# Performance work log

Measured on AMD Instinct MI355X. Metric: run time of the kernel, lower is better.

The kernel has to match this reference:

```python
import jax, jax.numpy as jnp
import numpy as np

N = 50000
E = 800000
D_IN = 128
HID = 128
L = 3


def setup_inputs() -> dict:
    key = jax.random.key(0)
    ks = jax.random.split(key, 16)
    s = 0.05
    return {
        "x": jax.random.normal(ks[0], (N, D_IN), jnp.float32),
        "edge_attr": jax.random.normal(ks[1], (E, 1), jnp.float32),
        "edge_index": jax.random.randint(ks[2], (2, E), 0, N, jnp.int64),
        # stacked per-layer GINEConv params (all layers have in=out=128)
        "Wl1": jax.random.normal(ks[3], (L, D_IN, HID), jnp.float32) * s,
        "bl1": jax.random.normal(ks[4], (L, HID), jnp.float32) * s,
        "Wl2": jax.random.normal(ks[5], (L, HID, HID), jnp.float32) * s,
        "bl2": jax.random.normal(ks[6], (L, HID), jnp.float32) * s,
        # edge_attr linear: edge_dim=1 -> in_channels of each layer's nn
        "We": jax.random.normal(ks[7], (L, 1, D_IN), jnp.float32) * s,
        "be": jax.random.normal(ks[8], (L, D_IN), jnp.float32) * s,
        # edge predictor MLP: Linear(2*HID, HID) -> ReLU -> (Dropout: eval) -> Linear(HID, 1)
        "Wp1": jax.random.normal(ks[9], (2 * HID, HID), jnp.float32) * s,
        "bp1": jax.random.normal(ks[10], (HID,), jnp.float32) * s,
        "Wp2": jax.random.normal(ks[11], (HID, 1), jnp.float32) * s,
        "bp2": jax.random.normal(ks[12], (1,), jnp.float32) * s,
    }


def reference(x, edge_attr, edge_index, Wl1, bl1, Wl2, bl2, We, be, Wp1, bp1, Wp2, bp2):
    src, dst = edge_index[0], edge_index[1]  # PyG: row=source j, col=target i
    n = x.shape[0]
    for l in range(Wl1.shape[0]):
        # GINEConv message: ReLU(x_j + Lin(edge_attr)); sum-aggregate into target i
        msg = jax.nn.relu(x[src] + edge_attr @ We[l] + be[l])        # [E, D]
        aggr = jax.ops.segment_sum(msg, dst, num_segments=n)         # [N, D]
        # out = nn((1+eps)*x + aggr), eps=0; nn = Lin->ReLU->Lin; then outer ReLU
        h = jax.nn.relu((x + aggr) @ Wl1[l] + bl1[l])
        x = jax.nn.relu(h @ Wl2[l] + bl2[l])
    edge_feat = jnp.concatenate([x[src], x[dst]], axis=1)            # [E, 2*HID]
    h = jax.nn.relu(edge_feat @ Wp1 + bp1)                           # dropout = identity (eval)
    return (h @ Wp2 + bp2).squeeze(-1)                               # [E]
```

## Files before the change

kernel.cpp:

```cpp
#include <hip/hip_runtime.h>

#define NN 50000
#define NE 800000
#define DD 128

typedef __attribute__((ext_vector_type(8))) short short8;
typedef __attribute__((ext_vector_type(4))) float f32x4;

__device__ inline unsigned short f2bf_rne(float f) {
  unsigned u = __float_as_uint(f);
  u += 0x7FFF + ((u >> 16) & 1);
  return (unsigned short)(u >> 16);
}
__device__ inline float bf2f(unsigned short h) {
  return __uint_as_float(((unsigned)h) << 16);
}

__global__ __launch_bounds__(256) void prologue(
    const float* __restrict__ Wl1, const float* __restrict__ Wl2,
    const float* __restrict__ Wp1,
    unsigned short* __restrict__ WTh, unsigned short* __restrict__ WTl,
    const float2* __restrict__ xin2, unsigned* __restrict__ xbf2,
    int* __restrict__ cnt) {
  const int tid = blockIdx.x * 256 + threadIdx.x;
  if (tid < NN) cnt[tid] = 0;
  if (tid < 8 * 16384) {
    const int g = tid >> 14, idx = tid & 16383;
    const int n = idx >> 7, k = idx & 127;
    const float* s;
    if (g < 3) s = Wl1 + (size_t)g * 16384;
    else if (g < 6) s = Wl2 + (size_t)(g - 3) * 16384;
    else s = Wp1 + (size_t)(g - 6) * 16384;
    const float v = s[k * 128 + n];
    const unsigned short hi = f2bf_rne(v);
    WTh[tid] = hi;
    WTl[tid] = f2bf_rne(v - bf2f(hi));
  }
  if (tid < NN * DD / 2) {
    const float2 v = xin2[tid];
    xbf2[tid] = (unsigned)f2bf_rne(v.x) | ((unsigned)f2bf_rne(v.y) << 16);
  }
}

__global__ __launch_bounds__(256) void hist_rank(const int* __restrict__ dst,
                                                 int* __restrict__ cnt,
                                                 int* __restrict__ rank) {
  int e = blockIdx.x * 256 + threadIdx.x;
  if (e < NE) rank[e] = atomicAdd(&cnt[dst[e]], 1);
}

__global__ __launch_bounds__(1024) void scan_nodes(const int* __restrict__ cnt,
                                                   int* __restrict__ offs) {
  __shared__ int wsum[16];
  __shared__ int wpre[16];
  const int t = threadIdx.x;
  const int lane = t & 63, wv = t >> 6;
  int carry = 0;
  for (int base = 0; base < NN; base += 8192) {
    const int i0 = base + t * 8;
    int4 a = make_int4(0, 0, 0, 0), b = make_int4(0, 0, 0, 0);
    if (i0 + 8 <= NN) {
      a = *(const int4*)(cnt + i0);
      b = *(const int4*)(cnt + i0 + 4);
    } else if (i0 < NN) {
      int tmp[8];
      for (int j = 0; j < 8; ++j) tmp[j] = (i0 + j < NN) ? cnt[i0 + j] : 0;
      a = make_int4(tmp[0], tmp[1], tmp[2], tmp[3]);
      b = make_int4(tmp[4], tmp[5], tmp[6], tmp[7]);
    }
    const int own = a.x + a.y + a.z + a.w + b.x + b.y + b.z + b.w;
    int inc = own;
#pragma unroll
    for (int d = 1; d < 64; d <<= 1) {
      int v = __shfl_up(inc, d, 64);
      if (lane >= d) inc += v;
    }
    if (lane == 63) wsum[wv] = inc;
    __syncthreads();
    if (t < 16) {
      int v = wsum[t];
      int p = v;
#pragma unroll
      for (int d = 1; d < 16; d <<= 1) {
        int u = __shfl_up(p, d, 16);
        if (t >= d) p += u;
      }
      wpre[t] = p - v;
      if (t == 15) wsum[15] = p;
    }
    __syncthreads();
    int run = carry + wpre[wv] + inc - own;
    const int o0 = run,      o1 = o0 + a.x, o2 = o1 + a.y, o3 = o2 + a.z;
    const int o4 = o3 + a.w, o5 = o4 + b.x, o6 = o5 + b.y, o7 = o6 + b.z;
    if (i0 + 8 <= NN) {
      *(int4*)(offs + i0)     = make_int4(o0, o1, o2, o3);
      *(int4*)(offs + i0 + 4) = make_int4(o4, o5, o6, o7);
    } else if (i0 < NN) {
      const int o[8] = {o0, o1, o2, o3, o4, o5, o6, o7};
      for (int j = 0; j < 8; ++j)
        if (i0 + j < NN) offs[i0 + j] = o[j];
    }
    carry += wsum[15];
    __syncthreads();
  }
  if (t == 0) offs[NN] = carry;
}

__global__ __launch_bounds__(256) void csr_fill(
    const int* __restrict__ src, const int* __restrict__ dst,
    const float* __restrict__ ea, const int* __restrict__ offs,
    const int* __restrict__ rank, int4* __restrict__ recs) {
  int e = blockIdx.x * 256 + threadIdx.x;
  if (e >= NE) return;
  int pos = offs[dst[e]] + rank[e];
  recs[pos] = make_int4(src[e], e, __float_as_int(ea[e]), 0);
}

__global__ __launch_bounds__(256) void aggregate(
    const unsigned short* __restrict__ xbf,
    const int* __restrict__ offs, const int4* __restrict__ recs,
    const float4* __restrict__ We4, const float4* __restrict__ be4,
    float* __restrict__ out) {
  const int slot = threadIdx.x >> 5, lane = threadIdx.x & 31;
  const int n = blockIdx.x * 8 + slot;
  if (n >= NN) return;
  const float4 wv = We4[lane], bv = be4[lane];
  const uint2 sq = *(const uint2*)(xbf + (size_t)n * DD + lane * 4);
  float4 a0, a1, a2, a3;
  a0.x = __uint_as_float(sq.x << 16);
  a0.y = __uint_as_float(sq.x & 0xffff0000u);
  a0.z = __uint_as_float(sq.y << 16);
  a0.w = __uint_as_float(sq.y & 0xffff0000u);
  a1 = make_float4(0.f, 0.f, 0.f, 0.f);
  a2 = make_float4(0.f, 0.f, 0.f, 0.f);
  a3 = make_float4(0.f, 0.f, 0.f, 0.f);
  const int beg = offs[n], end = offs[n + 1];
  int i = beg;
#define ACCQ(acc, rec, qq)                                                    \
  {                                                                           \
    const float ee = __int_as_float((rec).z);                                 \
    const float g0 = __uint_as_float((qq).x << 16);                           \
    const float g1 = __uint_as_float((qq).x & 0xffff0000u);                   \
    const float g2 = __uint_as_float((qq).y << 16);                           \
    const float g3 = __uint_as_float((qq).y & 0xffff0000u);                   \
    acc.x += fmaxf(fmaf(ee, wv.x, bv.x) + g0, 0.f);                           \
    acc.y += fmaxf(fmaf(ee, wv.y, bv.y) + g1, 0.f);                           \
    acc.z += fmaxf(fmaf(ee, wv.z, bv.z) + g2, 0.f);                           \
    acc.w += fmaxf(fmaf(ee, wv.w, bv.w) + g3, 0.f);                           \
  }
  for (; i + 8 <= end; i += 8) {
    int4 r[8];
#pragma unroll
    for (int u = 0; u < 8; ++u) r[u] = recs[i + u];
    uint2 q[8];
#pragma unroll
    for (int u = 0; u < 8; ++u)
      q[u] = *(const uint2*)(xbf + (size_t)r[u].x * DD + lane * 4);
    ACCQ(a0, r[0], q[0]) ACCQ(a1, r[1], q[1]) ACCQ(a2, r[2], q[2]) ACCQ(a3, r[3], q[3])
    ACCQ(a0, r[4], q[4]) ACCQ(a1, r[5], q[5]) ACCQ(a2, r[6], q[6]) ACCQ(a3, r[7], q[7])
  }
  for (; i + 4 <= end; i += 4) {
    int4 r[4];
#pragma unroll
    for (int u = 0; u < 4; ++u) r[u] = recs[i + u];
    uint2 q[4];
#pragma unroll
    for (int u = 0; u < 4; ++u)
      q[u] = *(const uint2*)(xbf + (size_t)r[u].x * DD + lane * 4);
    ACCQ(a0, r[0], q[0]) ACCQ(a1, r[1], q[1]) ACCQ(a2, r[2], q[2]) ACCQ(a3, r[3], q[3])
  }
  for (; i < end; ++i) {
    const int4 r0 = recs[i];
    const uint2 q0 = *(const uint2*)(xbf + (size_t)r0.x * DD + lane * 4);
    ACCQ(a0, r0, q0)
  }
#undef ACCQ
  a0.x += a1.x + a2.x + a3.x;
  a0.y += a1.y + a2.y + a3.y;
  a0.z += a1.z + a2.z + a3.z;
  a0.w += a1.w + a2.w + a3.w;
  ((float4*)(out + (size_t)n * DD))[lane] = a0;
}

template <bool F32OUT, bool BFOUT>
__global__ __launch_bounds__(256) void fused_mlp(
    const float* __restrict__ in,
    const unsigned short* __restrict__ W1h, const unsigned short* __restrict__ W1l,
    const unsigned short* __restrict__ W2h, const unsigned short* __restrict__ W2l,
    const float* __restrict__ b1, const float* __restrict__ b2,
    float* __restrict__ out, unsigned short* __restrict__ outbf) {
  __shared__ float hl[16][132];
  const int t = threadIdx.x;
  const int w = t >> 6, l = t & 63;
  const int lr = l & 15, kg = l >> 4;

  short8 B1h_[2][4], B1l_[2][4], B2h_[2][4], B2l_[2][4];
#pragma unroll
  for (int ct = 0; ct < 2; ++ct)
#pragma unroll
    for (int ks = 0; ks < 4; ++ks) {
      const size_t bo = (size_t)((w * 2 + ct) * 16 + lr) * DD + ks * 32 + kg * 8;
      B1h_[ct][ks] = *(const short8*)(W1h + bo);
      B1l_[ct][ks] = *(const short8*)(W1l + bo);
      B2h_[ct][ks] = *(const short8*)(W2h + bo);
      B2l_[ct][ks] = *(const short8*)(W2l + bo);
    }
  const float b1v0 = b1[(w * 2 + 0) * 16 + lr];
  const float b1v1 = b1[(w * 2 + 1) * 16 + lr];
  const float b2v0 = b2[(w * 2 + 0) * 16 + lr];
  const float b2v1 = b2[(w * 2 + 1) * 16 + lr];

  for (int c = blockIdx.x; c < NN / 16; c += gridDim.x) {
    f32x4 acc[2];
    {
      const float* ap = in + ((size_t)c * 16 + lr) * DD + kg * 8;
      float va[4][8];
#pragma unroll
      for (int ks = 0; ks < 4; ++ks) {
        *(float4*)&va[ks][0] = *(const float4*)(ap + ks * 32);
        *(float4*)&va[ks][4] = *(const float4*)(ap + ks * 32 + 4);
      }
      short8 ah[4], al[4];
#pragma unroll
      for (int ks = 0; ks < 4; ++ks)
#pragma unroll
        for (int j = 0; j < 8; ++j) {
          unsigned short h = f2bf_rne(va[ks][j]);
          ah[ks][j] = (short)h;
          al[ks][j] = (short)f2bf_rne(va[ks][j] - bf2f(h));
        }
      acc[0] = (f32x4){0.f, 0.f, 0.f, 0.f};
      acc[1] = (f32x4){0.f, 0.f, 0.f, 0.f};
#pragma unroll
      for (int ks = 0; ks < 4; ++ks)
#pragma unroll
        for (int ct = 0; ct < 2; ++ct) {
          acc[ct] = __builtin_amdgcn_mfma_f32_16x16x32_bf16(ah[ks], B1h_[ct][ks], acc[ct], 0, 0, 0);
          acc[ct] = __builtin_amdgcn_mfma_f32_16x16x32_bf16(ah[ks], B1l_[ct][ks], acc[ct], 0, 0, 0);
          acc[ct] = __builtin_amdgcn_mfma_f32_16x16x32_bf16(al[ks], B1h_[ct][ks], acc[ct], 0, 0, 0);
        }
    }
    __syncthreads();
#pragma unroll
    for (int ct = 0; ct < 2; ++ct) {
      const float bb = ct ? b1v1 : b1v0;
      const int col = (w * 2 + ct) * 16 + lr;
#pragma unroll
      for (int q = 0; q < 4; ++q)
        hl[kg * 4 + q][col] = fmaxf(acc[ct][q] + bb, 0.f);
    }
    __syncthreads();
    {
      float va[4][8];
#pragma unroll
      for (int ks = 0; ks < 4; ++ks) {
        *(float4*)&va[ks][0] = *(const float4*)&hl[lr][ks * 32 + kg * 8];
        *(float4*)&va[ks][4] = *(const float4*)&hl[lr][ks * 32 + kg * 8 + 4];
      }
      short8 ah[4], al[4];
#pragma unroll
      for (int ks = 0; ks < 4; ++ks)
#pragma unroll
        for (int j = 0; j < 8; ++j) {
          unsigned short h = f2bf_rne(va[ks][j]);
          ah[ks][j] = (short)h;
          al[ks][j] = (short)f2bf_rne(va[ks][j] - bf2f(h));
        }
      acc[0] = (f32x4){0.f, 0.f, 0.f, 0.f};
      acc[1] = (f32x4){0.f, 0.f, 0.f, 0.f};
#pragma unroll
      for (int ks = 0; ks < 4; ++ks)
#pragma unroll
        for (int ct = 0; ct < 2; ++ct) {
          acc[ct] = __builtin_amdgcn_mfma_f32_16x16x32_bf16(ah[ks], B2h_[ct][ks], acc[ct], 0, 0, 0);
          acc[ct] = __builtin_amdgcn_mfma_f32_16x16x32_bf16(ah[ks], B2l_[ct][ks], acc[ct], 0, 0, 0);
          acc[ct] = __builtin_amdgcn_mfma_f32_16x16x32_bf16(al[ks], B2h_[ct][ks], acc[ct], 0, 0, 0);
        }
    }
#pragma unroll
    for (int ct = 0; ct < 2; ++ct) {
      const float bb = ct ? b2v1 : b2v0;
      const int col = (w * 2 + ct) * 16 + lr;
#pragma unroll
      for (int q = 0; q < 4; ++q) {
        const float v = fmaxf(acc[ct][q] + bb, 0.f);
        const size_t r = (size_t)c * 16 + kg * 4 + q;
        if (F32OUT) out[r * DD + col] = v;
        if (BFOUT) outbf[r * DD + col] = f2bf_rne(v);
      }
    }
  }
}

__global__ __launch_bounds__(256) void gemm_pred2(
    const float* __restrict__ in,
    const unsigned short* __restrict__ W1h, const unsigned short* __restrict__ W1l,
    const unsigned short* __restrict__ W2h, const unsigned short* __restrict__ W2l,
    const float* __restrict__ bp1,
    unsigned short* __restrict__ P1bf, unsigned short* __restrict__ P2bf) {
  const int t = threadIdx.x;
  const int w = t >> 6, l = t & 63;
  const int lr = l & 15, kg = l >> 4;

  short8 B1h[2][4], B1l[2][4], B2h[2][4], B2l[2][4];
#pragma unroll
  for (int ct = 0; ct < 2; ++ct)
#pragma unroll
    for (int ks = 0; ks < 4; ++ks) {
      const size_t bo = (size_t)((w * 2 + ct) * 16 + lr) * DD + ks * 32 + kg * 8;
      B1h[ct][ks] = *(const short8*)(W1h + bo);
      B1l[ct][ks] = *(const short8*)(W1l + bo);
      B2h[ct][ks] = *(const short8*)(W2h + bo);
      B2l[ct][ks] = *(const short8*)(W2l + bo);
    }
  float bv0 = bp1[(w * 2 + 0) * 16 + lr];
  float bv1 = bp1[(w * 2 + 1) * 16 + lr];

  for (int c = blockIdx.x; c < NN / 16; c += gridDim.x) {
    const float* ap = in + ((size_t)c * 16 + lr) * DD + kg * 8;
    float va[4][8];
#pragma unroll
    for (int ks = 0; ks < 4; ++ks) {
      *(float4*)&va[ks][0] = *(const float4*)(ap + ks * 32);
      *(float4*)&va[ks][4] = *(const float4*)(ap + ks * 32 + 4);
    }
    short8 ah[4], al[4];
#pragma unroll
    for (int ks = 0; ks < 4; ++ks)
#pragma unroll
      for (int j = 0; j < 8; ++j) {
        unsigned short h = f2bf_rne(va[ks][j]);
        ah[ks][j] = (short)h;
        al[ks][j] = (short)f2bf_rne(va[ks][j] - bf2f(h));
      }
    f32x4 acc1[2], acc2[2];
    acc1[0] = (f32x4){0.f, 0.f, 0.f, 0.f};
    acc1[1] = (f32x4){0.f, 0.f, 0.f, 0.f};
    acc2[0] = (f32x4){0.f, 0.f, 0.f, 0.f};
    acc2[1] = (f32x4){0.f, 0.f, 0.f, 0.f};
#pragma unroll
    for (int ks = 0; ks < 4; ++ks) {
#pragma unroll
      for (int ct = 0; ct < 2; ++ct) {
        acc1[ct] = __builtin_amdgcn_mfma_f32_16x16x32_bf16(ah[ks], B1h[ct][ks], acc1[ct], 0, 0, 0);
        acc1[ct] = __builtin_amdgcn_mfma_f32_16x16x32_bf16(ah[ks], B1l[ct][ks], acc1[ct], 0, 0, 0);
        acc1[ct] = __builtin_amdgcn_mfma_f32_16x16x32_bf16(al[ks], B1h[ct][ks], acc1[ct], 0, 0, 0);
        acc2[ct] = __builtin_amdgcn_mfma_f32_16x16x32_bf16(ah[ks], B2h[ct][ks], acc2[ct], 0, 0, 0);
        acc2[ct] = __builtin_amdgcn_mfma_f32_16x16x32_bf16(ah[ks], B2l[ct][ks], acc2[ct], 0, 0, 0);
        acc2[ct] = __builtin_amdgcn_mfma_f32_16x16x32_bf16(al[ks], B2h[ct][ks], acc2[ct], 0, 0, 0);
      }
    }
#pragma unroll
    for (int ct = 0; ct < 2; ++ct) {
      const int col = (w * 2 + ct) * 16 + lr;
      const float bb = ct ? bv1 : bv0;
#pragma unroll
      for (int q4 = 0; q4 < 4; ++q4) {
        const size_t r = (size_t)c * 16 + kg * 4 + q4;
        P1bf[r * DD + col] = f2bf_rne(acc1[ct][q4]);
        P2bf[r * DD + col] = f2bf_rne(acc2[ct][q4] + bb);
      }
    }
  }
}

__global__ __launch_bounds__(256) void edge_out(
    const unsigned short* __restrict__ P1bf, const unsigned short* __restrict__ P2bf,
    const int* __restrict__ offs, const int4* __restrict__ recs,
    const float4* __restrict__ Wp2_4,
    const float* __restrict__ bp2, float* __restrict__ out) {
  const int slot = threadIdx.x >> 5, lane = threadIdx.x & 31;
  const int n = blockIdx.x * 8 + slot;
  if (n >= NN) return;
  const float4 w = Wp2_4[lane];
  const float bb = bp2[0];
  const uint2 pq = *(const uint2*)(P2bf + (size_t)n * DD + lane * 4);
  float4 p2;
  p2.x = __uint_as_float(pq.x << 16);
  p2.y = __uint_as_float(pq.x & 0xffff0000u);
  p2.z = __uint_as_float(pq.y << 16);
  p2.w = __uint_as_float(pq.y & 0xffff0000u);
  const int beg = offs[n], end = offs[n + 1];
  int i = beg;
#define EDGEV(vv, qq)                                                         \
  {                                                                           \
    const float q0 = __uint_as_float((qq).x << 16);                           \
    const float q1 = __uint_as_float((qq).x & 0xffff0000u);                   \
    const float q2 = __uint_as_float((qq).y << 16);                           \
    const float q3 = __uint_as_float((qq).y & 0xffff0000u);                   \
    vv = fmaxf(q0 + p2.x, 0.f) * w.x + fmaxf(q1 + p2.y, 0.f) * w.y            \
       + fmaxf(q2 + p2.z, 0.f) * w.z + fmaxf(q3 + p2.w, 0.f) * w.w;           \
  }
  for (; i + 8 <= end; i += 8) {
    int4 r[8];
#pragma unroll
    for (int u = 0; u < 8; ++u) r[u] = recs[i + u];
    uint2 q[8];
#pragma unroll
    for (int u = 0; u < 8; ++u)
      q[u] = *(const uint2*)(P1bf + (size_t)r[u].x * DD + lane * 4);
    float v[8];
#pragma unroll
    for (int u = 0; u < 8; ++u) EDGEV(v[u], q[u])
#pragma unroll
    for (int m = 16; m >= 1; m >>= 1) {
#pragma unroll
      for (int u = 0; u < 8; ++u) v[u] += __shfl_xor(v[u], m, 64);
    }
    if (lane == 0) {
#pragma unroll
      for (int u = 0; u < 8; ++u) out[r[u].y] = v[u] + bb;
    }
  }
  for (; i + 4 <= end; i += 4) {
    int4 r[4];
#pragma unroll
    for (int u = 0; u < 4; ++u) r[u] = recs[i + u];
    uint2 q[4];
#pragma unroll
    for (int u = 0; u < 4; ++u)
      q[u] = *(const uint2*)(P1bf + (size_t)r[u].x * DD + lane * 4);
    float v[4];
#pragma unroll
    for (int u = 0; u < 4; ++u) EDGEV(v[u], q[u])
#pragma unroll
    for (int m = 16; m >= 1; m >>= 1) {
#pragma unroll
      for (int u = 0; u < 4; ++u) v[u] += __shfl_xor(v[u], m, 64);
    }
    if (lane == 0) {
#pragma unroll
      for (int u = 0; u < 4; ++u) out[r[u].y] = v[u] + bb;
    }
  }
  for (; i < end; ++i) {
    const int4 rec = recs[i];
    const uint2 qq = *(const uint2*)(P1bf + (size_t)rec.x * DD + lane * 4);
    float v;
    EDGEV(v, qq)
#pragma unroll
    for (int m = 16; m >= 1; m >>= 1) v += __shfl_xor(v, m, 64);
    if (lane == 0) out[rec.y] = v + bb;
  }
#undef EDGEV
}

extern "C" void kernel_launch(void* const* d_in, const int* in_sizes, int n_in,
                              void* d_out, int out_size, void* d_ws, size_t ws_size,
                              hipStream_t stream) {
  const float* x_in = (const float*)d_in[0];
  const float* ea   = (const float*)d_in[1];
  const int*   ei   = (const int*)d_in[2];
  const float* Wl1 = (const float*)d_in[3];
  const float* bl1 = (const float*)d_in[4];
  const float* Wl2 = (const float*)d_in[5];
  const float* bl2 = (const float*)d_in[6];
  const float* We  = (const float*)d_in[7];
  const float* be  = (const float*)d_in[8];
  const float* Wp1 = (const float*)d_in[9];
  const float* bp1 = (const float*)d_in[10];
  const float* Wp2 = (const float*)d_in[11];
  const float* bp2 = (const float*)d_in[12];
  const int* src = ei;
  const int* dst = ei + NE;

  float* bufA   = (float*)d_ws;
  float* bufB   = bufA + (size_t)NN * DD;
  int*   cnt    = (int*)(bufB + (size_t)NN * DD);
  int*   offs   = cnt + NN;
  int*   rank   = offs + NN + 1;
  int4*  recs   = (int4*)(((uintptr_t)(rank + NE) + 15) & ~(uintptr_t)15);
  unsigned short* WTh = (unsigned short*)(recs + NE);
  unsigned short* WTl = WTh + 8 * 16384;
  unsigned short* xbf = WTl + 8 * 16384;

  prologue<<<(NN * DD / 2 + 255) / 256, 256, 0, stream>>>(
      Wl1, Wl2, Wp1, WTh, WTl, (const float2*)x_in, (unsigned*)xbf, cnt);
  hist_rank<<<NE / 256, 256, 0, stream>>>(dst, cnt, rank);
  scan_nodes<<<1, 1024, 0, stream>>>(cnt, offs);
  csr_fill<<<NE / 256, 256, 0, stream>>>(src, dst, ea, offs, rank, recs);

  const int GB = 1024;
  const int AB = (NN + 7) / 8;
#define WH(g) (WTh + (size_t)(g) * 16384)
#define WL(g) (WTl + (size_t)(g) * 16384)

  aggregate<<<AB, 256, 0, stream>>>(
      xbf, offs, recs, (const float4*)We, (const float4*)be, bufA);
  fused_mlp<false, true><<<GB, 256, 0, stream>>>(
      bufA, WH(0), WL(0), WH(3), WL(3), bl1, bl2, nullptr, xbf);
  aggregate<<<AB, 256, 0, stream>>>(
      xbf, offs, recs, (const float4*)(We + DD), (const float4*)(be + DD), bufA);
  fused_mlp<false, true><<<GB, 256, 0, stream>>>(
      bufA, WH(1), WL(1), WH(4), WL(4), bl1 + DD, bl2 + DD, nullptr, xbf);
  aggregate<<<AB, 256, 0, stream>>>(
      xbf, offs, recs, (const float4*)(We + 2 * DD), (const float4*)(be + 2 * DD), bufA);
  fused_mlp<true, false><<<GB, 256, 0, stream>>>(
      bufA, WH(2), WL(2), WH(5), WL(5), bl1 + 2 * DD, bl2 + 2 * DD, bufB, nullptr);
  gemm_pred2<<<GB, 256, 0, stream>>>(bufB, WH(6), WL(6), WH(7), WL(7), bp1,
                                     (unsigned short*)bufA, xbf);
  edge_out<<<AB, 256, 0, stream>>>(
      (const unsigned short*)bufA, xbf, offs, recs,
      (const float4*)Wp2, bp2, (float*)d_out);
}
```

Baseline: 386.1 us.

## Pack CSR records into 8 bytes and gather rows with 16-lane, 16-byte loads

Shrinks each CSR record from an int4 to a uint2. The record packs a 16-bit source index, a 32-bit edge id split across both words, and the edge attribute rounded to bf16. This halves the record traffic read by the three aggregate passes and by edge_out. Both gather kernels also now map 16 lanes per node with 128-bit loads instead of 32 lanes with 64-bit loads, so each block handles 16 nodes and edge_out needs a shorter shuffle reduction. In exchange, the edge attribute loses precision, and the packing relies on N fitting in 16 bits.

Measured after the change: 390.0 us. About the same (+1.0%).

```diff
diff --git a/kernel.cpp b/kernel.cpp
--- a/kernel.cpp
+++ b/kernel.cpp
@@ -15,6 +15,8 @@
 __device__ inline float bf2f(unsigned short h) {
   return __uint_as_float(((unsigned)h) << 16);
 }
+__device__ inline float bflo(unsigned u) { return __uint_as_float(u << 16); }
+__device__ inline float bfhi(unsigned u) { return __uint_as_float(u & 0xffff0000u); }
 
 __global__ __launch_bounds__(256) void prologue(
     const float* __restrict__ Wl1, const float* __restrict__ Wl2,
@@ -109,77 +111,79 @@
 __global__ __launch_bounds__(256) void csr_fill(
     const int* __restrict__ src, const int* __restrict__ dst,
     const float* __restrict__ ea, const int* __restrict__ offs,
-    const int* __restrict__ rank, int4* __restrict__ recs) {
+    const int* __restrict__ rank, uint2* __restrict__ recs) {
   int e = blockIdx.x * 256 + threadIdx.x;
   if (e >= NE) return;
   int pos = offs[dst[e]] + rank[e];
-  recs[pos] = make_int4(src[e], e, __float_as_int(ea[e]), 0);
+  const unsigned s = (unsigned)src[e];
+  const unsigned eb = (unsigned)f2bf_rne(ea[e]);
+  recs[pos] = make_uint2(s | ((unsigned)e << 16),
+                         ((unsigned)e >> 16) | (eb << 16));
 }
 
 __global__ __launch_bounds__(256) void aggregate(
     const unsigned short* __restrict__ xbf,
-    const int* __restrict__ offs, const int4* __restrict__ recs,
+    const int* __restrict__ offs, const uint2* __restrict__ recs,
     const float4* __restrict__ We4, const float4* __restrict__ be4,
     float* __restrict__ out) {
-  const int slot = threadIdx.x >> 5, lane = threadIdx.x & 31;
-  const int n = blockIdx.x * 8 + slot;
+  const int slot = threadIdx.x >> 4, lane = threadIdx.x & 15;
+  const int n = blockIdx.x * 16 + slot;
   if (n >= NN) return;
-  const float4 wv = We4[lane], bv = be4[lane];
-  const uint2 sq = *(const uint2*)(xbf + (size_t)n * DD + lane * 4);
-  float4 a0, a1, a2, a3;
-  a0.x = __uint_as_float(sq.x << 16);
-  a0.y = __uint_as_float(sq.x & 0xffff0000u);
-  a0.z = __uint_as_float(sq.y << 16);
-  a0.w = __uint_as_float(sq.y & 0xffff0000u);
-  a1 = make_float4(0.f, 0.f, 0.f, 0.f);
-  a2 = make_float4(0.f, 0.f, 0.f, 0.f);
-  a3 = make_float4(0.f, 0.f, 0.f, 0.f);
+  const float4 wv0 = We4[lane * 2], wv1 = We4[lane * 2 + 1];
+  const float4 bv0 = be4[lane * 2], bv1 = be4[lane * 2 + 1];
+  float acc[8];
+  {
+    const uint4 sq = *(const uint4*)(xbf + (size_t)n * DD + lane * 8);
+    acc[0] = bflo(sq.x); acc[1] = bfhi(sq.x);
+    acc[2] = bflo(sq.y); acc[3] = bfhi(sq.y);
+    acc[4] = bflo(sq.z); acc[5] = bfhi(sq.z);
+    acc[6] = bflo(sq.w); acc[7] = bfhi(sq.w);
+  }
   const int beg = offs[n], end = offs[n + 1];
   int i = beg;
-#define ACCQ(acc, rec, qq)                                                    \
+#define ACC8(rec, q)                                                          \
   {                                                                           \
-    const float ee = __int_as_float((rec).z);                                 \
-    const float g0 = __uint_as_float((qq).x << 16);                           \
-    const float g1 = __uint_as_float((qq).x & 0xffff0000u);                   \
-    const float g2 = __uint_as_float((qq).y << 16);                           \
-    const float g3 = __uint_as_float((qq).y & 0xffff0000u);                   \
-    acc.x += fmaxf(fmaf(ee, wv.x, bv.x) + g0, 0.f);                           \
-    acc.y += fmaxf(fmaf(ee, wv.y, bv.y) + g1, 0.f);                           \
-    acc.z += fmaxf(fmaf(ee, wv.z, bv.z) + g2, 0.f);                           \
-    acc.w += fmaxf(fmaf(ee, wv.w, bv.w) + g3, 0.f);                           \
+    const float ee = bf2f((unsigned short)((rec).y >> 16));                   \
+    acc[0] += fmaxf(fmaf(ee, wv0.x, bv0.x) + bflo((q).x), 0.f);               \
+    acc[1] += fmaxf(fmaf(ee, wv0.y, bv0.y) + bfhi((q).x), 0.f);               \
+    acc[2] += fmaxf(fmaf(ee, wv0.z, bv0.z) + bflo((q).y), 0.f);               \
+    acc[3] += fmaxf(fmaf(ee, wv0.w, bv0.w) + bfhi((q).y), 0.f);               \
+    acc[4] += fmaxf(fmaf(ee, wv1.x, bv1.x) + bflo((q).z), 0.f);               \
+    acc[5] += fmaxf(fmaf(ee, wv1.y, bv1.y) + bfhi((q).z), 0.f);               \
+    acc[6] += fmaxf(fmaf(ee, wv1.z, bv1.z) + bflo((q).w), 0.f);               \
+    acc[7] += fmaxf(fmaf(ee, wv1.w, bv1.w) + bfhi((q).w), 0.f);               \
   }
   for (; i + 8 <= end; i += 8) {
-    int4 r[8];
+    uint2 r[8];
 #pragma unroll
     for (int u = 0; u < 8; ++u) r[u] = recs[i + u];
-    uint2 q[8];
+    uint4 q[8];
 #pragma unroll
     for (int u = 0; u < 8; ++u)
-      q[u] = *(const uint2*)(xbf + (size_t)r[u].x * DD + lane * 4);
-    ACCQ(a0, r[0], q[0]) ACCQ(a1, r[1], q[1]) ACCQ(a2, r[2], q[2]) ACCQ(a3, r[3], q[3])
-    ACCQ(a0, r[4], q[4]) ACCQ(a1, r[5], q[5]) ACCQ(a2, r[6], q[6]) ACCQ(a3, r[7], q[7])
+      q[u] = *(const uint4*)(xbf + (size_t)(r[u].x & 0xFFFFu) * DD + lane * 8);
+#pragma unroll
+    for (int u = 0; u < 8; ++u) ACC8(r[u], q[u])
   }
   for (; i + 4 <= end; i += 4) {
-    int4 r[4];
+    uint2 r[4];
 #pragma unroll
     for (int u = 0; u < 4; ++u) r[u] = recs[i + u];
-    uint2 q[4];
+    uint4 q[4];
 #pragma unroll
     for (int u = 0; u < 4; ++u)
-      q[u] = *(const uint2*)(xbf + (size_t)r[u].x * DD + lane * 4);
-    ACCQ(a0, r[0], q[0]) ACCQ(a1, r[1], q[1]) ACCQ(a2, r[2], q[2]) ACCQ(a3, r[3], q[3])
+      q[u] = *(const uint4*)(xbf + (size_t)(r[u].x & 0xFFFFu) * DD + lane * 8);
+#pragma unroll
+    for (int u = 0; u < 4; ++u) ACC8(r[u], q[u])
   }
   for (; i < end; ++i) {
-    const int4 r0 = recs[i];
-    const uint2 q0 = *(const uint2*)(xbf + (size_t)r0.x * DD + lane * 4);
-    ACCQ(a0, r0, q0)
-  }
-#undef ACCQ
-  a0.x += a1.x + a2.x + a3.x;
-  a0.y += a1.y + a2.y + a3.y;
-  a0.z += a1.z + a2.z + a3.z;
-  a0.w += a1.w + a2.w + a3.w;
-  ((float4*)(out + (size_t)n * DD))[lane] = a0;
+    const uint2 r0 = recs[i];
+    const uint4 q0 = *(const uint4*)(xbf + (size_t)(r0.x & 0xFFFFu) * DD + lane * 8);
+    ACC8(r0, q0)
+  }
+#undef ACC8
+  float* orow = out + (size_t)n * DD + lane * 8;
+  *(float4*)orow = make_float4(acc[0], acc[1], acc[2], acc[3]);
+  *(float4*)(orow + 4) = make_float4(acc[4], acc[5], acc[6], acc[7]);
 }
 
 template <bool F32OUT, bool BFOUT>
@@ -366,83 +370,89 @@
 
 __global__ __launch_bounds__(256) void edge_out(
     const unsigned short* __restrict__ P1bf, const unsigned short* __restrict__ P2bf,
-    const int* __restrict__ offs, const int4* __restrict__ recs,
+    const int* __restrict__ offs, const uint2* __restrict__ recs,
     const float4* __restrict__ Wp2_4,
     const float* __restrict__ bp2, float* __restrict__ out) {
-  const int slot = threadIdx.x >> 5, lane = threadIdx.x & 31;
-  const int n = blockIdx.x * 8 + slot;
+  const int slot = threadIdx.x >> 4, lane = threadIdx.x & 15;
+  const int n = blockIdx.x * 16 + slot;
   if (n >= NN) return;
-  const float4 w = Wp2_4[lane];
+  const float4 w0 = Wp2_4[lane * 2], w1 = Wp2_4[lane * 2 + 1];
   const float bb = bp2[0];
-  const uint2 pq = *(const uint2*)(P2bf + (size_t)n * DD + lane * 4);
-  float4 p2;
-  p2.x = __uint_as_float(pq.x << 16);
-  p2.y = __uint_as_float(pq.x & 0xffff0000u);
-  p2.z = __uint_as_float(pq.y << 16);
-  p2.w = __uint_as_float(pq.y & 0xffff0000u);
+  float p[8];
+  {
+    const uint4 pq = *(const uint4*)(P2bf + (size_t)n * DD + lane * 8);
+    p[0] = bflo(pq.x); p[1] = bfhi(pq.x);
+    p[2] = bflo(pq.y); p[3] = bfhi(pq.y);
+    p[4] = bflo(pq.z); p[5] = bfhi(pq.z);
+    p[6] = bflo(pq.w); p[7] = bfhi(pq.w);
+  }
   const int beg = offs[n], end = offs[n + 1];
   int i = beg;
-#define EDGEV(vv, qq)                                                         \
+#define EDGEV(vv, q)                                                          \
   {                                                                           \
-    const float q0 = __uint_as_float((qq).x << 16);                           \
-    const float q1 = __uint_as_float((qq).x & 0xffff0000u);                   \
-    const float q2 = __uint_as_float((qq).y << 16);                           \
-    const float q3 = __uint_as_float((qq).y & 0xffff0000u);                   \
-    vv = fmaxf(q0 + p2.x, 0.f) * w.x + fmaxf(q1 + p2.y, 0.f) * w.y            \
-       + fmaxf(q2 + p2.z, 0.f) * w.z + fmaxf(q3 + p2.w, 0.f) * w.w;           \
-  }
+    vv = fmaxf(bflo((q).x) + p[0], 0.f) * w0.x                                \
+       + fmaxf(bfhi((q).x) + p[1], 0.f) * w0.y                                \
+       + fmaxf(bflo((q).y) + p[2], 0.f) * w0.z                                \
+       + fmaxf(bfhi((q).y) + p[3], 0.f) * w0.w                                \
+       + fmaxf(bflo((q).z) + p[4], 0.f) * w1.x                                \
+       + fmaxf(bfhi((q).z) + p[5], 0.f) * w1.y                                \
+       + fmaxf(bflo((q).w) + p[6], 0.f) * w1.z                                \
+       + fmaxf(bfhi((q).w) + p[7], 0.f) * w1.w;                               \
+  }
+#define EID(r) (((r).x >> 16) | (((r).y & 0xFFFFu) << 16))
   for (; i + 8 <= end; i += 8) {
-    int4 r[8];
+    uint2 r[8];
 #pragma unroll
     for (int u = 0; u < 8; ++u) r[u] = recs[i + u];
-    uint2 q[8];
+    uint4 q[8];
 #pragma unroll
     for (int u = 0; u < 8; ++u)
-      q[u] = *(const uint2*)(P1bf + (size_t)r[u].x * DD + lane * 4);
+      q[u] = *(const uint4*)(P1bf + (size_t)(r[u].x & 0xFFFFu) * DD + lane * 8);
     float v[8];
 #pragma unroll
     for (int u = 0; u < 8; ++u) EDGEV(v[u], q[u])
 #pragma unroll
-    for (int m = 16; m >= 1; m >>= 1) {
+    for (int m = 8; m >= 1; m >>= 1) {
 #pragma unroll
       for (int u = 0; u < 8; ++u) v[u] += __shfl_xor(v[u], m, 64);
     }
     if (lane == 0) {
 #pragma unroll
-      for (int u = 0; u < 8; ++u) out[r[u].y] = v[u] + bb;
+      for (int u = 0; u < 8; ++u) out[EID(r[u])] = v[u] + bb;
     }
   }
   for (; i + 4 <= end; i += 4) {
-    int4 r[4];
+    uint2 r[4];
 #pragma unroll
     for (int u = 0; u < 4; ++u) r[u] = recs[i + u];
-    uint2 q[4];
+    uint4 q[4];
 #pragma unroll
     for (int u = 0; u < 4; ++u)
-      q[u] = *(const uint2*)(P1bf + (size_t)r[u].x * DD + lane * 4);
+      q[u] = *(const uint4*)(P1bf + (size_t)(r[u].x & 0xFFFFu) * DD + lane * 8);
     float v[4];
 #pragma unroll
     for (int u = 0; u < 4; ++u) EDGEV(v[u], q[u])
 #pragma unroll
-    for (int m = 16; m >= 1; m >>= 1) {
+    for (int m = 8; m >= 1; m >>= 1) {
 #pragma unroll
       for (int u = 0; u < 4; ++u) v[u] += __shfl_xor(v[u], m, 64);
     }
     if (lane == 0) {
 #pragma unroll
-      for (int u = 0; u < 4; ++u) out[r[u].y] = v[u] + bb;
+      for (int u = 0; u < 4; ++u) out[EID(r[u])] = v[u] + bb;
     }
   }
   for (; i < end; ++i) {
-    const int4 rec = recs[i];
-    const uint2 qq = *(const uint2*)(P1bf + (size_t)rec.x * DD + lane * 4);
+    const uint2 r0 = recs[i];
+    const uint4 q0 = *(const uint4*)(P1bf + (size_t)(r0.x & 0xFFFFu) * DD + lane * 8);
     float v;
-    EDGEV(v, qq)
-#pragma unroll
-    for (int m = 16; m >= 1; m >>= 1) v += __shfl_xor(v, m, 64);
-    if (lane == 0) out[rec.y] = v + bb;
+    EDGEV(v, q0)
+#pragma unroll
+    for (int m = 8; m >= 1; m >>= 1) v += __shfl_xor(v, m, 64);
+    if (lane == 0) out[EID(r0)] = v + bb;
   }
 #undef EDGEV
+#undef EID
 }
 
 extern "C" void kernel_launch(void* const* d_in, const int* in_sizes, int n_in,
@@ -469,7 +479,7 @@
   int*   cnt    = (int*)(bufB + (size_t)NN * DD);
   int*   offs   = cnt + NN;
   int*   rank   = offs + NN + 1;
-  int4*  recs   = (int4*)(((uintptr_t)(rank + NE) + 15) & ~(uintptr_t)15);
+  uint2* recs   = (uint2*)(((uintptr_t)(rank + NE) + 15) & ~(uintptr_t)15);
   unsigned short* WTh = (unsigned short*)(recs + NE);
   unsigned short* WTl = WTh + 8 * 16384;
   unsigned short* xbf = WTl + 8 * 16384;
@@ -481,7 +491,7 @@
   csr_fill<<<NE / 256, 256, 0, stream>>>(src, dst, ea, offs, rank, recs);
 
   const int GB = 1024;
-  const int AB = (NN + 7) / 8;
+  const int AB = (NN + 15) / 16;
 #define WH(g) (WTh + (size_t)(g) * 16384)
 #define WL(g) (WTl + (size_t)(g) * 16384)
 
```

## Pack CSR records to 8 bytes and store aggregates and activations as bf16

Applied to the files above, without the earlier changes.

CSR records shrink from int4 to uint2, packing a 16-bit source index, a 32-bit edge id split across both words, and the bf16 edge attribute. Aggregate outputs and the final-layer activations are now written as bf16, so the MLP and predictor GEMMs load bf16 directly. This drops the hi/lo split of activations and one of the three MFMA passes per split-precision product. The aim is to cut memory traffic and MFMA work, at the cost of precision. The 16-bit source field only holds because N=50000 fits in 16 bits, and it truncates larger node ids.

Measured after the change: 355.6 us. 1.09x faster.

```diff
diff --git a/kernel.cpp b/kernel.cpp
--- a/kernel.cpp
+++ b/kernel.cpp
@@ -15,6 +15,8 @@
 __device__ inline float bf2f(unsigned short h) {
   return __uint_as_float(((unsigned)h) << 16);
 }
+__device__ inline float bflo(unsigned u) { return __uint_as_float(u << 16); }
+__device__ inline float bfhi(unsigned u) { return __uint_as_float(u & 0xffff0000u); }
 
 __global__ __launch_bounds__(256) void prologue(
     const float* __restrict__ Wl1, const float* __restrict__ Wl2,
@@ -109,28 +111,31 @@
 __global__ __launch_bounds__(256) void csr_fill(
     const int* __restrict__ src, const int* __restrict__ dst,
     const float* __restrict__ ea, const int* __restrict__ offs,
-    const int* __restrict__ rank, int4* __restrict__ recs) {
+    const int* __restrict__ rank, uint2* __restrict__ recs) {
   int e = blockIdx.x * 256 + threadIdx.x;
   if (e >= NE) return;
   int pos = offs[dst[e]] + rank[e];
-  recs[pos] = make_int4(src[e], e, __float_as_int(ea[e]), 0);
+  const unsigned s = (unsigned)src[e];
+  const unsigned eb = (unsigned)f2bf_rne(ea[e]);
+  recs[pos] = make_uint2(s | ((unsigned)e << 16),
+                         ((unsigned)e >> 16) | (eb << 16));
 }
 
 __global__ __launch_bounds__(256) void aggregate(
     const unsigned short* __restrict__ xbf,
-    const int* __restrict__ offs, const int4* __restrict__ recs,
+    const int* __restrict__ offs, const uint2* __restrict__ recs,
     const float4* __restrict__ We4, const float4* __restrict__ be4,
-    float* __restrict__ out) {
+    unsigned* __restrict__ outbf2) {
   const int slot = threadIdx.x >> 5, lane = threadIdx.x & 31;
   const int n = blockIdx.x * 8 + slot;
   if (n >= NN) return;
   const float4 wv = We4[lane], bv = be4[lane];
-  const uint2 sq = *(const uint2*)(xbf + (size_t)n * DD + lane * 4);
   float4 a0, a1, a2, a3;
-  a0.x = __uint_as_float(sq.x << 16);
-  a0.y = __uint_as_float(sq.x & 0xffff0000u);
-  a0.z = __uint_as_float(sq.y << 16);
-  a0.w = __uint_as_float(sq.y & 0xffff0000u);
+  {
+    const uint2 sq = *(const uint2*)(xbf + (size_t)n * DD + lane * 4);
+    a0.x = bflo(sq.x); a0.y = bfhi(sq.x);
+    a0.z = bflo(sq.y); a0.w = bfhi(sq.y);
+  }
   a1 = make_float4(0.f, 0.f, 0.f, 0.f);
   a2 = make_float4(0.f, 0.f, 0.f, 0.f);
   a3 = make_float4(0.f, 0.f, 0.f, 0.f);
@@ -138,40 +143,36 @@
   int i = beg;
 #define ACCQ(acc, rec, qq)                                                    \
   {                                                                           \
-    const float ee = __int_as_float((rec).z);                                 \
-    const float g0 = __uint_as_float((qq).x << 16);                           \
-    const float g1 = __uint_as_float((qq).x & 0xffff0000u);                   \
-    const float g2 = __uint_as_float((qq).y << 16);                           \
-    const float g3 = __uint_as_float((qq).y & 0xffff0000u);                   \
-    acc.x += fmaxf(fmaf(ee, wv.x, bv.x) + g0, 0.f);                           \
-    acc.y += fmaxf(fmaf(ee, wv.y, bv.y) + g1, 0.f);                           \
-    acc.z += fmaxf(fmaf(ee, wv.z, bv.z) + g2, 0.f);                           \
-    acc.w += fmaxf(fmaf(ee, wv.w, bv.w) + g3, 0.f);                           \
+    const float ee = bf2f((unsigned short)((rec).y >> 16));                   \
+    acc.x += fmaxf(fmaf(ee, wv.x, bv.x) + bflo((qq).x), 0.f);                 \
+    acc.y += fmaxf(fmaf(ee, wv.y, bv.y) + bfhi((qq).x), 0.f);                 \
+    acc.z += fmaxf(fmaf(ee, wv.z, bv.z) + bflo((qq).y), 0.f);                 \
+    acc.w += fmaxf(fmaf(ee, wv.w, bv.w) + bfhi((qq).y), 0.f);                 \
   }
   for (; i + 8 <= end; i += 8) {
-    int4 r[8];
+    uint2 r[8];
 #pragma unroll
     for (int u = 0; u < 8; ++u) r[u] = recs[i + u];
     uint2 q[8];
 #pragma unroll
     for (int u = 0; u < 8; ++u)
-      q[u] = *(const uint2*)(xbf + (size_t)r[u].x * DD + lane * 4);
+      q[u] = *(const uint2*)(xbf + (size_t)(r[u].x & 0xFFFFu) * DD + lane * 4);
     ACCQ(a0, r[0], q[0]) ACCQ(a1, r[1], q[1]) ACCQ(a2, r[2], q[2]) ACCQ(a3, r[3], q[3])
     ACCQ(a0, r[4], q[4]) ACCQ(a1, r[5], q[5]) ACCQ(a2, r[6], q[6]) ACCQ(a3, r[7], q[7])
   }
   for (; i + 4 <= end; i += 4) {
-    int4 r[4];
+    uint2 r[4];
 #pragma unroll
     for (int u = 0; u < 4; ++u) r[u] = recs[i + u];
     uint2 q[4];
 #pragma unroll
     for (int u = 0; u < 4; ++u)
-      q[u] = *(const uint2*)(xbf + (size_t)r[u].x * DD + lane * 4);
+      q[u] = *(const uint2*)(xbf + (size_t)(r[u].x & 0xFFFFu) * DD + lane * 4);
     ACCQ(a0, r[0], q[0]) ACCQ(a1, r[1], q[1]) ACCQ(a2, r[2], q[2]) ACCQ(a3, r[3], q[3])
   }
   for (; i < end; ++i) {
-    const int4 r0 = recs[i];
-    const uint2 q0 = *(const uint2*)(xbf + (size_t)r0.x * DD + lane * 4);
+    const uint2 r0 = recs[i];
+    const uint2 q0 = *(const uint2*)(xbf + (size_t)(r0.x & 0xFFFFu) * DD + lane * 4);
     ACCQ(a0, r0, q0)
   }
 #undef ACCQ
@@ -179,16 +180,18 @@
   a0.y += a1.y + a2.y + a3.y;
   a0.z += a1.z + a2.z + a3.z;
   a0.w += a1.w + a2.w + a3.w;
-  ((float4*)(out + (size_t)n * DD))[lane] = a0;
-}
-
-template <bool F32OUT, bool BFOUT>
+  const unsigned lo = (unsigned)f2bf_rne(a0.x) | ((unsigned)f2bf_rne(a0.y) << 16);
+  const unsigned hi = (unsigned)f2bf_rne(a0.z) | ((unsigned)f2bf_rne(a0.w) << 16);
+  uint2* orow = (uint2*)(outbf2 + (size_t)n * (DD / 2)) + lane;
+  *orow = make_uint2(lo, hi);
+}
+
 __global__ __launch_bounds__(256) void fused_mlp(
-    const float* __restrict__ in,
+    const unsigned short* __restrict__ in,
     const unsigned short* __restrict__ W1h, const unsigned short* __restrict__ W1l,
     const unsigned short* __restrict__ W2h, const unsigned short* __restrict__ W2l,
     const float* __restrict__ b1, const float* __restrict__ b2,
-    float* __restrict__ out, unsigned short* __restrict__ outbf) {
+    unsigned short* __restrict__ outbf) {
   __shared__ float hl[16][132];
   const int t = threadIdx.x;
   const int w = t >> 6, l = t & 63;
@@ -213,12 +216,36 @@
   for (int c = blockIdx.x; c < NN / 16; c += gridDim.x) {
     f32x4 acc[2];
     {
-      const float* ap = in + ((size_t)c * 16 + lr) * DD + kg * 8;
+      const unsigned short* ap = in + ((size_t)c * 16 + lr) * DD + kg * 8;
+      short8 ah[4];
+#pragma unroll
+      for (int ks = 0; ks < 4; ++ks) ah[ks] = *(const short8*)(ap + ks * 32);
+      acc[0] = (f32x4){0.f, 0.f, 0.f, 0.f};
+      acc[1] = (f32x4){0.f, 0.f, 0.f, 0.f};
+#pragma unroll
+      for (int ks = 0; ks < 4; ++ks)
+#pragma unroll
+        for (int ct = 0; ct < 2; ++ct) {
+          acc[ct] = __builtin_amdgcn_mfma_f32_16x16x32_bf16(ah[ks], B1h_[ct][ks], acc[ct], 0, 0, 0);
+          acc[ct] = __builtin_amdgcn_mfma_f32_16x16x32_bf16(ah[ks], B1l_[ct][ks], acc[ct], 0, 0, 0);
+        }
+    }
+    __syncthreads();
+#pragma unroll
+    for (int ct = 0; ct < 2; ++ct) {
+      const float bb = ct ? b1v1 : b1v0;
+      const int col = (w * 2 + ct) * 16 + lr;
+#pragma unroll
+      for (int q = 0; q < 4; ++q)
+        hl[kg * 4 + q][col] = fmaxf(acc[ct][q] + bb, 0.f);
+    }
+    __syncthreads();
+    {
       float va[4][8];
 #pragma unroll
       for (int ks = 0; ks < 4; ++ks) {
-        *(float4*)&va[ks][0] = *(const float4*)(ap + ks * 32);
-        *(float4*)&va[ks][4] = *(const float4*)(ap + ks * 32 + 4);
+        *(float4*)&va[ks][0] = *(const float4*)&hl[lr][ks * 32 + kg * 8];
+        *(float4*)&va[ks][4] = *(const float4*)&hl[lr][ks * 32 + kg * 8 + 4];
       }
       short8 ah[4], al[4];
 #pragma unroll
@@ -235,43 +262,6 @@
       for (int ks = 0; ks < 4; ++ks)
 #pragma unroll
         for (int ct = 0; ct < 2; ++ct) {
-          acc[ct] = __builtin_amdgcn_mfma_f32_16x16x32_bf16(ah[ks], B1h_[ct][ks], acc[ct], 0, 0, 0);
-          acc[ct] = __builtin_amdgcn_mfma_f32_16x16x32_bf16(ah[ks], B1l_[ct][ks], acc[ct], 0, 0, 0);
-          acc[ct] = __builtin_amdgcn_mfma_f32_16x16x32_bf16(al[ks], B1h_[ct][ks], acc[ct], 0, 0, 0);
-        }
-    }
-    __syncthreads();
-#pragma unroll
-    for (int ct = 0; ct < 2; ++ct) {
-      const float bb = ct ? b1v1 : b1v0;
-      const int col = (w * 2 + ct) * 16 + lr;
-#pragma unroll
-      for (int q = 0; q < 4; ++q)
-        hl[kg * 4 + q][col] = fmaxf(acc[ct][q] + bb, 0.f);
-    }
-    __syncthreads();
-    {
-      float va[4][8];
-#pragma unroll
-      for (int ks = 0; ks < 4; ++ks) {
-        *(float4*)&va[ks][0] = *(const float4*)&hl[lr][ks * 32 + kg * 8];
-        *(float4*)&va[ks][4] = *(const float4*)&hl[lr][ks * 32 + kg * 8 + 4];
-      }
-      short8 ah[4], al[4];
-#pragma unroll
-      for (int ks = 0; ks < 4; ++ks)
-#pragma unroll
-        for (int j = 0; j < 8; ++j) {
-          unsigned short h = f2bf_rne(va[ks][j]);
-          ah[ks][j] = (short)h;
-          al[ks][j] = (short)f2bf_rne(va[ks][j] - bf2f(h));
-        }
-      acc[0] = (f32x4){0.f, 0.f, 0.f, 0.f};
-      acc[1] = (f32x4){0.f, 0.f, 0.f, 0.f};
-#pragma unroll
-      for (int ks = 0; ks < 4; ++ks)
-#pragma unroll
-        for (int ct = 0; ct < 2; ++ct) {
           acc[ct] = __builtin_amdgcn_mfma_f32_16x16x32_bf16(ah[ks], B2h_[ct][ks], acc[ct], 0, 0, 0);
           acc[ct] = __builtin_amdgcn_mfma_f32_16x16x32_bf16(ah[ks], B2l_[ct][ks], acc[ct], 0, 0, 0);
           acc[ct] = __builtin_amdgcn_mfma_f32_16x16x32_bf16(al[ks], B2h_[ct][ks], acc[ct], 0, 0, 0);
@@ -284,16 +274,14 @@
 #pragma unroll
       for (int q = 0; q < 4; ++q) {
         const float v = fmaxf(acc[ct][q] + bb, 0.f);
-        const size_t r = (size_t)c * 16 + kg * 4 + q;
-        if (F32OUT) out[r * DD + col] = v;
-        if (BFOUT) outbf[r * DD + col] = f2bf_rne(v);
+        outbf[((size_t)c * 16 + kg * 4 + q) * DD + col] = f2bf_rne(v);
       }
     }
   }
 }
 
 __global__ __launch_bounds__(256) void gemm_pred2(
-    const float* __restrict__ in,
+    const unsigned short* __restrict__ in,
     const unsigned short* __restrict__ W1h, const unsigned short* __restrict__ W1l,
     const unsigned short* __restrict__ W2h, const unsigned short* __restrict__ W2l,
     const float* __restrict__ bp1,
@@ -317,22 +305,10 @@
   float bv1 = bp1[(w * 2 + 1) * 16 + lr];
 
   for (int c = blockIdx.x; c < NN / 16; c += gridDim.x) {
-    const float* ap = in + ((size_t)c * 16 + lr) * DD + kg * 8;
-    float va[4][8];
-#pragma unroll
-    for (int ks = 0; ks < 4; ++ks) {
-      *(float4*)&va[ks][0] = *(const float4*)(ap + ks * 32);
-      *(float4*)&va[ks][4] = *(const float4*)(ap + ks * 32 + 4);
-    }
-    short8 ah[4], al[4];
-#pragma unroll
-    for (int ks = 0; ks < 4; ++ks)
-#pragma unroll
-      for (int j = 0; j < 8; ++j) {
-        unsigned short h = f2bf_rne(va[ks][j]);
-        ah[ks][j] = (short)h;
-        al[ks][j] = (short)f2bf_rne(va[ks][j] - bf2f(h));
-      }
+    const unsigned short* ap = in + ((size_t)c * 16 + lr) * DD + kg * 8;
+    short8 ah[4];
+#pragma unroll
+    for (int ks = 0; ks < 4; ++ks) ah[ks] = *(const short8*)(ap + ks * 32);
     f32x4 acc1[2], acc2[2];
     acc1[0] = (f32x4){0.f, 0.f, 0.f, 0.f};
     acc1[1] = (f32x4){0.f, 0.f, 0.f, 0.f};
@@ -344,10 +320,8 @@
       for (int ct = 0; ct < 2; ++ct) {
         acc1[ct] = __builtin_amdgcn_mfma_f32_16x16x32_bf16(ah[ks], B1h[ct][ks], acc1[ct], 0, 0, 0);
         acc1[ct] = __builtin_amdgcn_mfma_f32_16x16x32_bf16(ah[ks], B1l[ct][ks], acc1[ct], 0, 0, 0);
-        acc1[ct] = __builtin_amdgcn_mfma_f32_16x16x32_bf16(al[ks], B1h[ct][ks], acc1[ct], 0, 0, 0);
         acc2[ct] = __builtin_amdgcn_mfma_f32_16x16x32_bf16(ah[ks], B2h[ct][ks], acc2[ct], 0, 0, 0);
         acc2[ct] = __builtin_amdgcn_mfma_f32_16x16x32_bf16(ah[ks], B2l[ct][ks], acc2[ct], 0, 0, 0);
-        acc2[ct] = __builtin_amdgcn_mfma_f32_16x16x32_bf16(al[ks], B2h[ct][ks], acc2[ct], 0, 0, 0);
       }
     }
 #pragma unroll
@@ -366,7 +340,7 @@
 
 __global__ __launch_bounds__(256) void edge_out(
     const unsigned short* __restrict__ P1bf, const unsigned short* __restrict__ P2bf,
-    const int* __restrict__ offs, const int4* __restrict__ recs,
+    const int* __restrict__ offs, const uint2* __restrict__ recs,
     const float4* __restrict__ Wp2_4,
     const float* __restrict__ bp2, float* __restrict__ out) {
   const int slot = threadIdx.x >> 5, lane = threadIdx.x & 31;
@@ -374,31 +348,30 @@
   if (n >= NN) return;
   const float4 w = Wp2_4[lane];
   const float bb = bp2[0];
-  const uint2 pq = *(const uint2*)(P2bf + (size_t)n * DD + lane * 4);
   float4 p2;
-  p2.x = __uint_as_float(pq.x << 16);
-  p2.y = __uint_as_float(pq.x & 0xffff0000u);
-  p2.z = __uint_as_float(pq.y << 16);
-  p2.w = __uint_as_float(pq.y & 0xffff0000u);
+  {
+    const uint2 pq = *(const uint2*)(P2bf + (size_t)n * DD + lane * 4);
+    p2.x = bflo(pq.x); p2.y = bfhi(pq.x);
+    p2.z = bflo(pq.y); p2.w = bfhi(pq.y);
+  }
   const int beg = offs[n], end = offs[n + 1];
   int i = beg;
 #define EDGEV(vv, qq)                                                         \
   {                                                                           \
-    const float q0 = __uint_as_float((qq).x << 16);                           \
-    const float q1 = __uint_as_float((qq).x & 0xffff0000u);                   \
-    const float q2 = __uint_as_float((qq).y << 16);                           \
-    const float q3 = __uint_as_float((qq).y & 0xffff0000u);                   \
-    vv = fmaxf(q0 + p2.x, 0.f) * w.x + fmaxf(q1 + p2.y, 0.f) * w.y            \
-       + fmaxf(q2 + p2.z, 0.f) * w.z + fmaxf(q3 + p2.w, 0.f) * w.w;           \
-  }
+    vv = fmaxf(bflo((qq).x) + p2.x, 0.f) * w.x                                \
+       + fmaxf(bfhi((qq).x) + p2.y, 0.f) * w.y                                \
+       + fmaxf(bflo((qq).y) + p2.z, 0.f) * w.z                                \
+       + fmaxf(bfhi((qq).y) + p2.w, 0.f) * w.w;                               \
+  }
+#define EID(r) (((r).x >> 16) | (((r).y & 0xFFFFu) << 16))
   for (; i + 8 <= end; i += 8) {
-    int4 r[8];
+    uint2 r[8];
 #pragma unroll
     for (int u = 0; u < 8; ++u) r[u] = recs[i + u];
     uint2 q[8];
 #pragma unroll
     for (int u = 0; u < 8; ++u)
-      q[u] = *(const uint2*)(P1bf + (size_t)r[u].x * DD + lane * 4);
+      q[u] = *(const uint2*)(P1bf + (size_t)(r[u].x & 0xFFFFu) * DD + lane * 4);
     float v[8];
 #pragma unroll
     for (int u = 0; u < 8; ++u) EDGEV(v[u], q[u])
@@ -409,17 +382,17 @@
     }
     if (lane == 0) {
 #pragma unroll
-      for (int u = 0; u < 8; ++u) out[r[u].y] = v[u] + bb;
+      for (int u = 0; u < 8; ++u) out[EID(r[u])] = v[u] + bb;
     }
   }
   for (; i + 4 <= end; i += 4) {
-    int4 r[4];
+    uint2 r[4];
 #pragma unroll
     for (int u = 0; u < 4; ++u) r[u] = recs[i + u];
     uint2 q[4];
 #pragma unroll
     for (int u = 0; u < 4; ++u)
-      q[u] = *(const uint2*)(P1bf + (size_t)r[u].x * DD + lane * 4);
+      q[u] = *(const uint2*)(P1bf + (size_t)(r[u].x & 0xFFFFu) * DD + lane * 4);
     float v[4];
 #pragma unroll
     for (int u = 0; u < 4; ++u) EDGEV(v[u], q[u])
@@ -430,19 +403,20 @@
     }
     if (lane == 0) {
 #pragma unroll
-      for (int u = 0; u < 4; ++u) out[r[u].y] = v[u] + bb;
+      for (int u = 0; u < 4; ++u) out[EID(r[u])] = v[u] + bb;
     }
   }
   for (; i < end; ++i) {
-    const int4 rec = recs[i];
-    const uint2 qq = *(const uint2*)(P1bf + (size_t)rec.x * DD + lane * 4);
+    const uint2 r0 = recs[i];
+    const uint2 q0 = *(const uint2*)(P1bf + (size_t)(r0.x & 0xFFFFu) * DD + lane * 4);
     float v;
-    EDGEV(v, qq)
+    EDGEV(v, q0)
 #pragma unroll
     for (int m = 16; m >= 1; m >>= 1) v += __shfl_xor(v, m, 64);
-    if (lane == 0) out[rec.y] = v + bb;
+    if (lane == 0) out[EID(r0)] = v + bb;
   }
 #undef EDGEV
+#undef EID
 }
 
 extern "C" void kernel_launch(void* const* d_in, const int* in_sizes, int n_in,
@@ -469,10 +443,12 @@
   int*   cnt    = (int*)(bufB + (size_t)NN * DD);
   int*   offs   = cnt + NN;
   int*   rank   = offs + NN + 1;
-  int4*  recs   = (int4*)(((uintptr_t)(rank + NE) + 15) & ~(uintptr_t)15);
+  uint2* recs   = (uint2*)(((uintptr_t)(rank + NE) + 15) & ~(uintptr_t)15);
   unsigned short* WTh = (unsigned short*)(recs + NE);
   unsigned short* WTl = WTh + 8 * 16384;
   unsigned short* xbf = WTl + 8 * 16384;
+  unsigned short* agg = (unsigned short*)bufA;
+  unsigned short* p2b = (unsigned short*)bufB;
 
   prologue<<<(NN * DD / 2 + 255) / 256, 256, 0, stream>>>(
       Wl1, Wl2, Wp1, WTh, WTl, (const float2*)x_in, (unsigned*)xbf, cnt);
@@ -486,20 +462,19 @@
 #define WL(g) (WTl + (size_t)(g) * 16384)
 
   aggregate<<<AB, 256, 0, stream>>>(
-      xbf, offs, recs, (const float4*)We, (const float4*)be, bufA);
-  fused_mlp<false, true><<<GB, 256, 0, stream>>>(
-      bufA, WH(0), WL(0), WH(3), WL(3), bl1, bl2, nullptr, xbf);
+      xbf, offs, recs, (const float4*)We, (const float4*)be, (unsigned*)agg);
+  fused_mlp<<<GB, 256, 0, stream>>>(
+      agg, WH(0), WL(0), WH(3), WL(3), bl1, bl2, xbf);
   aggregate<<<AB, 256, 0, stream>>>(
-      xbf, offs, recs, (const float4*)(We + DD), (const float4*)(be + DD), bufA);
-  fused_mlp<false, true><<<GB, 256, 0, stream>>>(
-      bufA, WH(1), WL(1), WH(4), WL(4), bl1 + DD, bl2 + DD, nullptr, xbf);
+      xbf, offs, recs, (const float4*)(We + DD), (const float4*)(be + DD), (unsigned*)agg);
+  fused_mlp<<<GB, 256, 0, stream>>>(
+      agg, WH(1), WL(1), WH(4), WL(4), bl1 + DD, bl2 + DD, xbf);
   aggregate<<<AB, 256, 0, stream>>>(
-      xbf, offs, recs, (const float4*)(We + 2 * DD), (const float4*)(be + 2 * DD), bufA);
-  fused_mlp<true, false><<<GB, 256, 0, stream>>>(
-      bufA, WH(2), WL(2), WH(5), WL(5), bl1 + 2 * DD, bl2 + 2 * DD, bufB, nullptr);
-  gemm_pred2<<<GB, 256, 0, stream>>>(bufB, WH(6), WL(6), WH(7), WL(7), bp1,
-                                     (unsigned short*)bufA, xbf);
+      xbf, offs, recs, (const float4*)(We + 2 * DD), (const float4*)(be + 2 * DD), (unsigned*)agg);
+  fused_mlp<<<GB, 256, 0, stream>>>(
+      agg, WH(2), WL(2), WH(5), WL(5), bl1 + 2 * DD, bl2 + 2 * DD, xbf);
+  gemm_pred2<<<GB, 256, 0, stream>>>(xbf, WH(6), WL(6), WH(7), WL(7), bp1,
+                                     agg, p2b);
   edge_out<<<AB, 256, 0, stream>>>(
-      (const unsigned short*)bufA, xbf, offs, recs,
-      (const float4*)Wp2, bp2, (float*)d_out);
-}
+      agg, p2b, offs, recs, (const float4*)Wp2, bp2, (float*)d_out);
+}
```
